# Kernel optimization log

Hardware: AMD Instinct MI355X
Metric: run time of the kernel (lower is better)

The kernel has to match this reference:

```python
import jax, jax.numpy as jnp
import numpy as np

N_NODES = 50000


def gcn_conv(x, W, b, src, dst, n):
    """PyG-style GCNConv: symmetric-normalized aggregation over A + I.
    x: [N, Fin], W: [Fin, Fout], b: [Fout], src/dst: [E] int edge endpoints.
    """
    h = x @ W  # [N, Fout]
    # degree with self-loops: deg[i] = 1 + in-degree(i)
    deg = jnp.zeros((n,), dtype=h.dtype).at[dst].add(1.0) + 1.0
    dinv = jax.lax.rsqrt(deg)  # deg^-1/2
    norm_e = dinv[src] * dinv[dst]  # [E]
    # message passing: sum_j norm_ij * h_j  (plus self-loop term deg_i^-1 * h_i)
    agg = jnp.zeros_like(h).at[dst].add(h[src] * norm_e[:, None])
    agg = agg + h * (dinv * dinv)[:, None]
    return agg + b


def setup_inputs() -> dict:
    key = jax.random.key(0)
    ks = jax.random.split(key, 9)
    N, F_in, H, C = N_NODES, 128, 64, 4
    E = 1600000
    node_features = jax.random.normal(ks[0], (N, F_in), dtype=jnp.float32)
    edge_index = jax.random.randint(ks[1], (2, E), 0, N, dtype=jnp.int32)
    s1 = 1.0 / np.sqrt(F_in)
    s2 = 1.0 / np.sqrt(H)
    W1 = jax.random.uniform(ks[2], (F_in, H), jnp.float32, -s1, s1)
    b1 = jax.random.uniform(ks[3], (H,), jnp.float32, -s1, s1)
    W2 = jax.random.uniform(ks[4], (H, H), jnp.float32, -s2, s2)
    b2 = jax.random.uniform(ks[5], (H,), jnp.float32, -s2, s2)
    W3 = jax.random.uniform(ks[6], (H, C), jnp.float32, -s2, s2)
    b3 = jax.random.uniform(ks[7], (C,), jnp.float32, -s2, s2)
    return {"node_features": node_features, "edge_index": edge_index,
            "W1": W1, "b1": b1, "W2": W2, "b2": b2, "W3": W3, "b3": b3}


def reference(node_features, edge_index, W1, b1, W2, b2, W3, b3):
    n = node_features.shape[0]
    src, dst = edge_index[0], edge_index[1]
    out = jax.nn.relu(gcn_conv(node_features, W1, b1, src, dst, n))
    # layer2 applied 7 times with SHARED weights (faithful to the source)
    for _ in range(7):
        out = jax.nn.relu(gcn_conv(out, W2, b2, src, dst, n))
    out = gcn_conv(out, W3, b3, src, dst, n)
    return jax.nn.softmax(out, axis=0)  # softmax over the node dimension (dim=0)
```

## Files before the change

kernel.cpp:

```cpp
#include <hip/hip_runtime.h>
#include <hip/hip_fp16.h>
#include <math.h>
#include <float.h>


#define NPART 8
#define BPP   104
#define T     4

typedef float f4 __attribute__((ext_vector_type(4)));


__global__ __launch_bounds__(256) void k_count(const int* __restrict__ src,
                                               const int* __restrict__ dst,
                                               unsigned* __restrict__ cnt,
                                               int E, int chunkS) {
    int e = blockIdx.x * 256 + threadIdx.x;
    if (e >= E) return;
    int d = dst[e];
    int t = src[e] / chunkS;
    atomicAdd(&cnt[d * T + t], 1u);
}

__global__ __launch_bounds__(256) void k_dinv(const int* __restrict__ rowt,
                                              float* __restrict__ dinv, int n) {
    int i = blockIdx.x * 256 + threadIdx.x;
    if (i < n) dinv[i] = rsqrtf(1.0f + (float)(rowt[i * T + T] - rowt[i * T]));
}


__global__ __launch_bounds__(256) void k_scan1(const unsigned* __restrict__ cnt,
                                               int* __restrict__ rowt,
                                               unsigned* __restrict__ bsum, int m) {
    __shared__ unsigned t[256];
    int i = blockIdx.x * 256 + threadIdx.x;
    unsigned v = (i < m) ? cnt[i] : 0u;
    t[threadIdx.x] = v;
    __syncthreads();
    #pragma unroll
    for (int off = 1; off < 256; off <<= 1) {
        unsigned u = (threadIdx.x >= (unsigned)off) ? t[threadIdx.x - off] : 0u;
        __syncthreads();
        t[threadIdx.x] += u;
        __syncthreads();
    }
    if (i < m) rowt[i] = (int)(t[threadIdx.x] - v);
    if (threadIdx.x == 255) bsum[blockIdx.x] = t[255];
}

__global__ __launch_bounds__(256) void k_scan2(unsigned* __restrict__ bsum,
                                               int* __restrict__ rowt,
                                               int nb, int m, int E) {
    __shared__ unsigned t[256];
    unsigned run = 0;
    for (int base = 0; base < nb; base += 256) {
        int i = base + threadIdx.x;
        unsigned v = (i < nb) ? bsum[i] : 0u;
        t[threadIdx.x] = v;
        __syncthreads();
        #pragma unroll
        for (int off = 1; off < 256; off <<= 1) {
            unsigned u = (threadIdx.x >= (unsigned)off) ? t[threadIdx.x - off] : 0u;
            __syncthreads();
            t[threadIdx.x] += u;
            __syncthreads();
        }
        if (i < nb) bsum[i] = run + t[threadIdx.x] - v;
        __syncthreads();
        run += t[255];
        __syncthreads();
    }
    if (threadIdx.x == 0) rowt[m] = E;
}

__global__ __launch_bounds__(256) void k_scan3(int* __restrict__ rowt,
                                               const unsigned* __restrict__ bsum, int m) {
    int i = blockIdx.x * 256 + threadIdx.x;
    if (i < m) rowt[i] += (int)bsum[blockIdx.x];
}


__global__ __launch_bounds__(256) void k_fill(const int* __restrict__ src,
                                              const int* __restrict__ dst,
                                              const int* __restrict__ rowt,
                                              unsigned* __restrict__ cursor,
                                              int* __restrict__ csr_src,
                                              int E, int chunk, int chunkS) {
    int part = blockIdx.x & (NPART - 1);
    int q = blockIdx.x >> 3;
    int lo = part * chunk, hi = lo + chunk;
    for (int e = q * 256 + threadIdx.x; e < E; e += 256 * BPP) {
        int d = dst[e];
        if (d >= lo && d < hi) {
            int s = src[e];
            int slot4 = d * T + s / chunkS;
            unsigned pos = atomicAdd(&cursor[slot4], 1u);
            csr_src[rowt[slot4] + (int)pos] = s;
        }
    }
}


__global__ __launch_bounds__(256) void k_gemm64_f32(const float* __restrict__ x,
                                                    const float* __restrict__ W,
                                                    const float* __restrict__ dinv,
                                                    __half* __restrict__ hs, int n) {
    __shared__ float Wl[128 * 64];
    {
        const f4* Wv = (const f4*)W;
        f4* Wlv = (f4*)Wl;
        for (int idx = threadIdx.x; idx < 128 * 16; idx += 256) Wlv[idx] = Wv[idx];
    }
    __syncthreads();
    int wave = threadIdx.x >> 6, lane = threadIdx.x & 63;
    int i0 = blockIdx.x * 16 + wave * 4;
    if (i0 >= n) return;
    if (i0 + 3 < n) {
        const f4* r0 = (const f4*)(x + (size_t)(i0 + 0) * 128);
        const f4* r1 = (const f4*)(x + (size_t)(i0 + 1) * 128);
        const f4* r2 = (const f4*)(x + (size_t)(i0 + 2) * 128);
        const f4* r3 = (const f4*)(x + (size_t)(i0 + 3) * 128);
        float a0 = 0.f, a1 = 0.f, a2 = 0.f, a3 = 0.f;
        #pragma unroll
        for (int k4 = 0; k4 < 32; ++k4) {
            f4 v0 = __builtin_nontemporal_load(&r0[k4]);
            f4 v1 = __builtin_nontemporal_load(&r1[k4]);
            f4 v2 = __builtin_nontemporal_load(&r2[k4]);
            f4 v3 = __builtin_nontemporal_load(&r3[k4]);
            float w0 = Wl[(k4 * 4 + 0) * 64 + lane];
            float w1 = Wl[(k4 * 4 + 1) * 64 + lane];
            float w2 = Wl[(k4 * 4 + 2) * 64 + lane];
            float w3 = Wl[(k4 * 4 + 3) * 64 + lane];
            a0 += v0.x * w0 + v0.y * w1 + v0.z * w2 + v0.w * w3;
            a1 += v1.x * w0 + v1.y * w1 + v1.z * w2 + v1.w * w3;
            a2 += v2.x * w0 + v2.y * w1 + v2.z * w2 + v2.w * w3;
            a3 += v3.x * w0 + v3.y * w1 + v3.z * w2 + v3.w * w3;
        }
        hs[(size_t)(i0 + 0) * 64 + lane] = __float2half(a0 * dinv[i0 + 0]);
        hs[(size_t)(i0 + 1) * 64 + lane] = __float2half(a1 * dinv[i0 + 1]);
        hs[(size_t)(i0 + 2) * 64 + lane] = __float2half(a2 * dinv[i0 + 2]);
        hs[(size_t)(i0 + 3) * 64 + lane] = __float2half(a3 * dinv[i0 + 3]);
    } else {
        for (int i = i0; i < n && i < i0 + 4; ++i) {
            const f4* r = (const f4*)(x + (size_t)i * 128);
            float acc = 0.f;
            #pragma unroll
            for (int k4 = 0; k4 < 32; ++k4) {
                f4 v = r[k4];
                acc += v.x * Wl[(k4 * 4 + 0) * 64 + lane];
                acc += v.y * Wl[(k4 * 4 + 1) * 64 + lane];
                acc += v.z * Wl[(k4 * 4 + 2) * 64 + lane];
                acc += v.w * Wl[(k4 * 4 + 3) * 64 + lane];
            }
            hs[(size_t)i * 64 + lane] = __float2half(acc * dinv[i]);
        }
    }
}


__global__ __launch_bounds__(256) void k_gemm64_f16(const __half* __restrict__ xh,
                                                    const float* __restrict__ W,
                                                    const float* __restrict__ dinv,
                                                    __half* __restrict__ hs, int n) {
    __shared__ float Wl[64 * 64];
    {
        const f4* Wv = (const f4*)W;
        f4* Wlv = (f4*)Wl;
        for (int idx = threadIdx.x; idx < 64 * 16; idx += 256) Wlv[idx] = Wv[idx];
    }
    __syncthreads();
    int wave = threadIdx.x >> 6, lane = threadIdx.x & 63;
    int i0 = blockIdx.x * 16 + wave * 4;
    if (i0 >= n) return;
    if (i0 + 3 < n) {
        const unsigned* r0 = (const unsigned*)(xh + (size_t)(i0 + 0) * 64);
        const unsigned* r1 = (const unsigned*)(xh + (size_t)(i0 + 1) * 64);
        const unsigned* r2 = (const unsigned*)(xh + (size_t)(i0 + 2) * 64);
        const unsigned* r3 = (const unsigned*)(xh + (size_t)(i0 + 3) * 64);
        float a0 = 0.f, a1 = 0.f, a2 = 0.f, a3 = 0.f;
        #pragma unroll
        for (int k2 = 0; k2 < 32; ++k2) {
            unsigned u0 = __builtin_nontemporal_load(&r0[k2]);
            unsigned u1 = __builtin_nontemporal_load(&r1[k2]);
            unsigned u2 = __builtin_nontemporal_load(&r2[k2]);
            unsigned u3 = __builtin_nontemporal_load(&r3[k2]);
            float w0 = Wl[(k2 * 2 + 0) * 64 + lane];
            float w1 = Wl[(k2 * 2 + 1) * 64 + lane];
            float2 v0 = __half22float2(*(__half2*)&u0);
            float2 v1 = __half22float2(*(__half2*)&u1);
            float2 v2 = __half22float2(*(__half2*)&u2);
            float2 v3 = __half22float2(*(__half2*)&u3);
            a0 += v0.x * w0 + v0.y * w1;
            a1 += v1.x * w0 + v1.y * w1;
            a2 += v2.x * w0 + v2.y * w1;
            a3 += v3.x * w0 + v3.y * w1;
        }
        hs[(size_t)(i0 + 0) * 64 + lane] = __float2half(a0 * dinv[i0 + 0]);
        hs[(size_t)(i0 + 1) * 64 + lane] = __float2half(a1 * dinv[i0 + 1]);
        hs[(size_t)(i0 + 2) * 64 + lane] = __float2half(a2 * dinv[i0 + 2]);
        hs[(size_t)(i0 + 3) * 64 + lane] = __float2half(a3 * dinv[i0 + 3]);
    } else {
        for (int i = i0; i < n && i < i0 + 4; ++i) {
            const __half2* r = (const __half2*)(xh + (size_t)i * 64);
            float acc = 0.f;
            #pragma unroll
            for (int k2 = 0; k2 < 32; ++k2) {
                float2 v = __half22float2(r[k2]);
                acc += v.x * Wl[(k2 * 2 + 0) * 64 + lane];
                acc += v.y * Wl[(k2 * 2 + 1) * 64 + lane];
            }
            hs[(size_t)i * 64 + lane] = __float2half(acc * dinv[i]);
        }
    }
}

__global__ __launch_bounds__(256) void k_gemm4(const __half* __restrict__ xh,
                                               const float* __restrict__ W,
                                               const float* __restrict__ dinv,
                                               float4* __restrict__ h4, int n) {
    __shared__ float Wl[256];
    for (int idx = threadIdx.x; idx < 256; idx += 256) Wl[idx] = W[idx];
    __syncthreads();
    int i = blockIdx.x * 256 + threadIdx.x;
    if (i >= n) return;
    const __half2* ar = (const __half2*)(xh + (size_t)i * 64);
    float a0 = 0.f, a1 = 0.f, a2 = 0.f, a3 = 0.f;
    #pragma unroll
    for (int k2 = 0; k2 < 32; ++k2) {
        float2 v = __half22float2(ar[k2]);
        int k = k2 * 2;
        a0 += v.x * Wl[k * 4 + 0] + v.y * Wl[(k + 1) * 4 + 0];
        a1 += v.x * Wl[k * 4 + 1] + v.y * Wl[(k + 1) * 4 + 1];
        a2 += v.x * Wl[k * 4 + 2] + v.y * Wl[(k + 1) * 4 + 2];
        a3 += v.x * Wl[k * 4 + 3] + v.y * Wl[(k + 1) * 4 + 3];
    }
    float di = dinv[i];
    h4[i] = make_float4(a0 * di, a1 * di, a2 * di, a3 * di);
}


__global__ __launch_bounds__(256) void k_agg64h(const __half* __restrict__ hs,
                                                const float* __restrict__ dinv,
                                                const int* __restrict__ rowt,
                                                const int* __restrict__ csr_src,
                                                const float* __restrict__ bias,
                                                __half* __restrict__ out, int n) {
    int wid = __builtin_amdgcn_readfirstlane((int)(threadIdx.x >> 6));
    int lane = threadIdx.x & 63;
    int gw = blockIdx.x * 4 + wid;
    if (gw >= n) return;
    float acc = __half2float(hs[(size_t)gw * 64 + lane]);
    int s = rowt[gw * T], e = rowt[gw * T + T];
    int slot = s;
    for (; slot + 16 <= e; slot += 16) {
        int idx[16];
        #pragma unroll
        for (int j = 0; j < 16; ++j) idx[j] = csr_src[slot + j];
        float v[16];
        #pragma unroll
        for (int j = 0; j < 16; ++j) v[j] = __half2float(hs[(size_t)idx[j] * 64 + lane]);
        float t0 = ((v[0] + v[1]) + (v[2] + v[3])) + ((v[4] + v[5]) + (v[6] + v[7]));
        float t1 = ((v[8] + v[9]) + (v[10] + v[11])) + ((v[12] + v[13]) + (v[14] + v[15]));
        acc += t0 + t1;
    }
    for (; slot + 4 <= e; slot += 4) {
        int i0 = csr_src[slot + 0];
        int i1 = csr_src[slot + 1];
        int i2 = csr_src[slot + 2];
        int i3 = csr_src[slot + 3];
        float v0 = __half2float(hs[(size_t)i0 * 64 + lane]);
        float v1 = __half2float(hs[(size_t)i1 * 64 + lane]);
        float v2 = __half2float(hs[(size_t)i2 * 64 + lane]);
        float v3 = __half2float(hs[(size_t)i3 * 64 + lane]);
        acc += (v0 + v1) + (v2 + v3);
    }
    for (; slot < e; ++slot)
        acc += __half2float(hs[(size_t)csr_src[slot] * 64 + lane]);
    acc = acc * dinv[gw] + bias[lane];
    out[(size_t)gw * 64 + lane] = __float2half(fmaxf(acc, 0.f));
}


__global__ __launch_bounds__(256) void k_agg4(const float4* __restrict__ h4,
                                              const float* __restrict__ dinv,
                                              const int* __restrict__ rowt,
                                              const int* __restrict__ csr_src,
                                              const float* __restrict__ b3,
                                              float4* __restrict__ z, int n) {
    int i = blockIdx.x * 256 + threadIdx.x;
    if (i >= n) return;
    float4 self = h4[i];
    float a0 = self.x, a1 = self.y, a2 = self.z, a3 = self.w;
    int s = rowt[i * T], e = rowt[i * T + T];
    int slot = s;
    for (; slot + 4 <= e; slot += 4) {
        int s0 = csr_src[slot + 0];
        int s1 = csr_src[slot + 1];
        int s2 = csr_src[slot + 2];
        int s3 = csr_src[slot + 3];
        float4 v0 = h4[s0], v1 = h4[s1], v2 = h4[s2], v3 = h4[s3];
        a0 += v0.x + v1.x + v2.x + v3.x;
        a1 += v0.y + v1.y + v2.y + v3.y;
        a2 += v0.z + v1.z + v2.z + v3.z;
        a3 += v0.w + v1.w + v2.w + v3.w;
    }
    for (; slot < e; ++slot) {
        float4 v = h4[csr_src[slot]];
        a0 += v.x; a1 += v.y; a2 += v.z; a3 += v.w;
    }
    float di = dinv[i];
    z[i] = make_float4(a0 * di + b3[0], a1 * di + b3[1],
                       a2 * di + b3[2], a3 * di + b3[3]);
}


__device__ inline unsigned encf(float f) {
    unsigned u = __float_as_uint(f);
    return (u & 0x80000000u) ? ~u : (u | 0x80000000u);
}
__device__ inline float decf(unsigned e) {
    return (e & 0x80000000u) ? __uint_as_float(e & 0x7FFFFFFFu) : __uint_as_float(~e);
}

__global__ __launch_bounds__(256) void k_max(const float4* __restrict__ z,
                                             unsigned* __restrict__ gmax, int n) {
    float m0 = -FLT_MAX, m1 = -FLT_MAX, m2 = -FLT_MAX, m3 = -FLT_MAX;
    for (int i = blockIdx.x * 256 + threadIdx.x; i < n; i += gridDim.x * 256) {
        float4 v = z[i];
        m0 = fmaxf(m0, v.x); m1 = fmaxf(m1, v.y);
        m2 = fmaxf(m2, v.z); m3 = fmaxf(m3, v.w);
    }
    #pragma unroll
    for (int off = 32; off; off >>= 1) {
        m0 = fmaxf(m0, __shfl_xor(m0, off));
        m1 = fmaxf(m1, __shfl_xor(m1, off));
        m2 = fmaxf(m2, __shfl_xor(m2, off));
        m3 = fmaxf(m3, __shfl_xor(m3, off));
    }
    if ((threadIdx.x & 63) == 0) {
        atomicMax(&gmax[0], encf(m0));
        atomicMax(&gmax[1], encf(m1));
        atomicMax(&gmax[2], encf(m2));
        atomicMax(&gmax[3], encf(m3));
    }
}

__global__ __launch_bounds__(256) void k_exp(const float4* __restrict__ z,
                                             float4* __restrict__ out,
                                             const unsigned* __restrict__ gmax,
                                             float* __restrict__ gsum, int n) {
    float M0 = decf(gmax[0]), M1 = decf(gmax[1]), M2 = decf(gmax[2]), M3 = decf(gmax[3]);
    float s0 = 0.f, s1 = 0.f, s2 = 0.f, s3 = 0.f;
    for (int i = blockIdx.x * 256 + threadIdx.x; i < n; i += gridDim.x * 256) {
        float4 v = z[i];
        float4 e;
        e.x = expf(v.x - M0); e.y = expf(v.y - M1);
        e.z = expf(v.z - M2); e.w = expf(v.w - M3);
        out[i] = e;
        s0 += e.x; s1 += e.y; s2 += e.z; s3 += e.w;
    }
    #pragma unroll
    for (int off = 32; off; off >>= 1) {
        s0 += __shfl_xor(s0, off);
        s1 += __shfl_xor(s1, off);
        s2 += __shfl_xor(s2, off);
        s3 += __shfl_xor(s3, off);
    }
    if ((threadIdx.x & 63) == 0) {
        atomicAdd(&gsum[0], s0);
        atomicAdd(&gsum[1], s1);
        atomicAdd(&gsum[2], s2);
        atomicAdd(&gsum[3], s3);
    }
}

__global__ __launch_bounds__(256) void k_norm(float4* __restrict__ out,
                                              const float* __restrict__ gsum, int n) {
    float r0 = 1.f / gsum[0], r1 = 1.f / gsum[1], r2 = 1.f / gsum[2], r3 = 1.f / gsum[3];
    for (int i = blockIdx.x * 256 + threadIdx.x; i < n; i += gridDim.x * 256) {
        float4 v = out[i];
        v.x *= r0; v.y *= r1; v.z *= r2; v.w *= r3;
        out[i] = v;
    }
}


extern "C" void kernel_launch(void* const* d_in, const int* in_sizes, int n_in,
                              void* d_out, int out_size, void* d_ws, size_t ws_size,
                              hipStream_t stream) {
    const float* x0 = (const float*)d_in[0];
    const int* ei = (const int*)d_in[1];
    const float* W1 = (const float*)d_in[2];
    const float* b1 = (const float*)d_in[3];
    const float* W2 = (const float*)d_in[4];
    const float* b2 = (const float*)d_in[5];
    const float* W3 = (const float*)d_in[6];
    const float* b3 = (const float*)d_in[7];

    const int n = in_sizes[0] / 128;
    const int E = in_sizes[1] / 2;
    const int* src = ei;
    const int* dst = ei + E;
    const int chunk = (n + NPART - 1) / NPART;
    const int chunkS = (n + T - 1) / T;
    const int m = n * T;

    char* ws = (char*)d_ws;
    size_t off = 0;
    auto alloc = [&](size_t bytes) -> void* {
        void* p = (void*)(ws + off);
        off = (off + bytes + 255) & ~(size_t)255;
        return p;
    };

    unsigned* cnt    = (unsigned*)alloc((size_t)m * 4);
    unsigned* cursor = (unsigned*)alloc((size_t)m * 4);
    unsigned* gmax   = (unsigned*)alloc(16);
    float*    gsum   = (float*)alloc(16);
    size_t zero_bytes = off;

    float* dinv      = (float*)alloc((size_t)n * 4);
    int*   rowt      = (int*)alloc((size_t)(m + 1) * 4);
    unsigned* bsum   = (unsigned*)alloc(1024 * 4);
    int*   csr_src   = (int*)alloc((size_t)E * 4);
    __half* hbuf     = (__half*)alloc((size_t)n * 64 * 2);
    __half* xbuf     = (__half*)alloc((size_t)n * 64 * 2);
    float4* h4buf    = (float4*)alloc((size_t)n * 16);
    float4* zbuf     = (float4*)alloc((size_t)n * 16);

    hipMemsetAsync(cnt, 0, zero_bytes, stream);

    const int nbN = (n + 255) / 256;
    const int nbE = (E + 255) / 256;
    const int nbM = (m + 255) / 256;

    k_count<<<nbE, 256, 0, stream>>>(src, dst, cnt, E, chunkS);
    k_scan1<<<nbM, 256, 0, stream>>>(cnt, rowt, bsum, m);
    k_scan2<<<1, 256, 0, stream>>>(bsum, rowt, nbM, m, E);
    k_scan3<<<nbM, 256, 0, stream>>>(rowt, bsum, m);
    k_dinv<<<nbN, 256, 0, stream>>>(rowt, dinv, n);
    k_fill<<<NPART * BPP, 256, 0, stream>>>(src, dst, rowt, cursor, csr_src, E, chunk, chunkS);

    const int nbG = (n + 15) / 16;
    const int nbA = (n + 3) / 4;

    k_gemm64_f32<<<nbG, 256, 0, stream>>>(x0, W1, dinv, hbuf, n);
    k_agg64h<<<nbA, 256, 0, stream>>>(hbuf, dinv, rowt, csr_src, b1, xbuf, n);

    for (int l = 0; l < 7; ++l) {
        k_gemm64_f16<<<nbG, 256, 0, stream>>>(xbuf, W2, dinv, hbuf, n);
        k_agg64h<<<nbA, 256, 0, stream>>>(hbuf, dinv, rowt, csr_src, b2, xbuf, n);
    }

    k_gemm4<<<nbN, 256, 0, stream>>>(xbuf, W3, dinv, h4buf, n);
    k_agg4<<<nbN, 256, 0, stream>>>(h4buf, dinv, rowt, csr_src, b3, zbuf, n);

    k_max<<<256, 256, 0, stream>>>(zbuf, gmax, n);
    k_exp<<<256, 256, 0, stream>>>(zbuf, (float4*)d_out, gmax, gsum, n);
    k_norm<<<256, 256, 0, stream>>>((float4*)d_out, gsum, n);
}
```

Measured before the change: 845.3 us.

## Compress CSR source indices to 16-bit pairs with even-padded segments

Stores the CSR neighbour indices as unsigned short instead of int, which halves the index traffic read in every aggregation pass. Each cell segment is padded to even length, and the pad slot points to an extra zero row at index n of the feature buffers. This lets the aggregation kernels read two indices per 32-bit load, and degree is now computed from the raw counts. The scheme relies on node ids fitting in 16 bits (N=50000) and adds a pad-fix kernel plus a zero-row kernel.

Measured after the change: 853.7 us. Within noise of the previous version (+1.0%).

```diff
diff --git a/kernel.cpp b/kernel.cpp
--- a/kernel.cpp
+++ b/kernel.cpp
@@ -22,10 +22,19 @@
     atomicAdd(&cnt[d * T + t], 1u);
 }
 
-__global__ __launch_bounds__(256) void k_dinv(const int* __restrict__ rowt,
+__global__ __launch_bounds__(256) void k_dinv(const unsigned* __restrict__ cnt,
                                               float* __restrict__ dinv, int n) {
     int i = blockIdx.x * 256 + threadIdx.x;
-    if (i < n) dinv[i] = rsqrtf(1.0f + (float)(rowt[i * T + T] - rowt[i * T]));
+    if (i < n) {
+        unsigned deg = cnt[i * T + 0] + cnt[i * T + 1] + cnt[i * T + 2] + cnt[i * T + 3];
+        dinv[i] = rsqrtf(1.0f + (float)deg);
+    }
+}
+
+__global__ __launch_bounds__(64) void k_zpad(__half* __restrict__ hs,
+                                             float4* __restrict__ h4, int n) {
+    hs[(size_t)n * 64 + threadIdx.x] = __float2half(0.f);
+    if (threadIdx.x == 0) h4[n] = make_float4(0.f, 0.f, 0.f, 0.f);
 }
 
 
@@ -34,7 +43,8 @@
                                                unsigned* __restrict__ bsum, int m) {
     __shared__ unsigned t[256];
     int i = blockIdx.x * 256 + threadIdx.x;
-    unsigned v = (i < m) ? cnt[i] : 0u;
+    unsigned v = 0;
+    if (i < m) { v = cnt[i]; v += (v & 1u); }
     t[threadIdx.x] = v;
     __syncthreads();
     #pragma unroll
@@ -50,7 +60,7 @@
 
 __global__ __launch_bounds__(256) void k_scan2(unsigned* __restrict__ bsum,
                                                int* __restrict__ rowt,
-                                               int nb, int m, int E) {
+                                               int nb, int m) {
     __shared__ unsigned t[256];
     unsigned run = 0;
     for (int base = 0; base < nb; base += 256) {
@@ -70,7 +80,7 @@
         run += t[255];
         __syncthreads();
     }
-    if (threadIdx.x == 0) rowt[m] = E;
+    if (threadIdx.x == 0) rowt[m] = (int)run;
 }
 
 __global__ __launch_bounds__(256) void k_scan3(int* __restrict__ rowt,
@@ -84,7 +94,7 @@
                                               const int* __restrict__ dst,
                                               const int* __restrict__ rowt,
                                               unsigned* __restrict__ cursor,
-                                              int* __restrict__ csr_src,
+                                              unsigned short* __restrict__ csr,
                                               int E, int chunk, int chunkS) {
     int part = blockIdx.x & (NPART - 1);
     int q = blockIdx.x >> 3;
@@ -93,11 +103,21 @@
         int d = dst[e];
         if (d >= lo && d < hi) {
             int s = src[e];
-            int slot4 = d * T + s / chunkS;
-            unsigned pos = atomicAdd(&cursor[slot4], 1u);
-            csr_src[rowt[slot4] + (int)pos] = s;
-        }
-    }
+            int cell = d * T + s / chunkS;
+            unsigned pos = atomicAdd(&cursor[cell], 1u);
+            csr[rowt[cell] + (int)pos] = (unsigned short)s;
+        }
+    }
+}
+
+__global__ __launch_bounds__(256) void k_padfix(const unsigned* __restrict__ cnt,
+                                                const int* __restrict__ rowt,
+                                                unsigned short* __restrict__ csr,
+                                                int m, int n) {
+    int i = blockIdx.x * 256 + threadIdx.x;
+    if (i >= m) return;
+    unsigned c = cnt[i];
+    if (c & 1u) csr[rowt[i] + (int)c] = (unsigned short)n;
 }
 
 
@@ -242,7 +262,7 @@
 __global__ __launch_bounds__(256) void k_agg64h(const __half* __restrict__ hs,
                                                 const float* __restrict__ dinv,
                                                 const int* __restrict__ rowt,
-                                                const int* __restrict__ csr_src,
+                                                const unsigned short* __restrict__ csr,
                                                 const float* __restrict__ bias,
                                                 __half* __restrict__ out, int n) {
     int wid = __builtin_amdgcn_readfirstlane((int)(threadIdx.x >> 6));
@@ -251,31 +271,28 @@
     if (gw >= n) return;
     float acc = __half2float(hs[(size_t)gw * 64 + lane]);
     int s = rowt[gw * T], e = rowt[gw * T + T];
-    int slot = s;
-    for (; slot + 16 <= e; slot += 16) {
-        int idx[16];
+    const unsigned* c32 = (const unsigned*)csr;
+    int p = s >> 1, pe = e >> 1;
+    for (; p + 8 <= pe; p += 8) {
+        unsigned pr[8];
         #pragma unroll
-        for (int j = 0; j < 16; ++j) idx[j] = csr_src[slot + j];
+        for (int j = 0; j < 8; ++j) pr[j] = c32[p + j];
         float v[16];
         #pragma unroll
-        for (int j = 0; j < 16; ++j) v[j] = __half2float(hs[(size_t)idx[j] * 64 + lane]);
+        for (int j = 0; j < 8; ++j) {
+            v[2 * j + 0] = __half2float(hs[(size_t)(pr[j] & 0xFFFFu) * 64 + lane]);
+            v[2 * j + 1] = __half2float(hs[(size_t)(pr[j] >> 16) * 64 + lane]);
+        }
         float t0 = ((v[0] + v[1]) + (v[2] + v[3])) + ((v[4] + v[5]) + (v[6] + v[7]));
         float t1 = ((v[8] + v[9]) + (v[10] + v[11])) + ((v[12] + v[13]) + (v[14] + v[15]));
         acc += t0 + t1;
     }
-    for (; slot + 4 <= e; slot += 4) {
-        int i0 = csr_src[slot + 0];
-        int i1 = csr_src[slot + 1];
-        int i2 = csr_src[slot + 2];
-        int i3 = csr_src[slot + 3];
-        float v0 = __half2float(hs[(size_t)i0 * 64 + lane]);
-        float v1 = __half2float(hs[(size_t)i1 * 64 + lane]);
-        float v2 = __half2float(hs[(size_t)i2 * 64 + lane]);
-        float v3 = __half2float(hs[(size_t)i3 * 64 + lane]);
-        acc += (v0 + v1) + (v2 + v3);
-    }
-    for (; slot < e; ++slot)
-        acc += __half2float(hs[(size_t)csr_src[slot] * 64 + lane]);
+    for (; p < pe; ++p) {
+        unsigned pr = c32[p];
+        float v0 = __half2float(hs[(size_t)(pr & 0xFFFFu) * 64 + lane]);
+        float v1 = __half2float(hs[(size_t)(pr >> 16) * 64 + lane]);
+        acc += v0 + v1;
+    }
     acc = acc * dinv[gw] + bias[lane];
     out[(size_t)gw * 64 + lane] = __float2half(fmaxf(acc, 0.f));
 }
@@ -284,7 +301,7 @@
 __global__ __launch_bounds__(256) void k_agg4(const float4* __restrict__ h4,
                                               const float* __restrict__ dinv,
                                               const int* __restrict__ rowt,
-                                              const int* __restrict__ csr_src,
+                                              const unsigned short* __restrict__ csr,
                                               const float* __restrict__ b3,
                                               float4* __restrict__ z, int n) {
     int i = blockIdx.x * 256 + threadIdx.x;
@@ -292,21 +309,22 @@
     float4 self = h4[i];
     float a0 = self.x, a1 = self.y, a2 = self.z, a3 = self.w;
     int s = rowt[i * T], e = rowt[i * T + T];
-    int slot = s;
-    for (; slot + 4 <= e; slot += 4) {
-        int s0 = csr_src[slot + 0];
-        int s1 = csr_src[slot + 1];
-        int s2 = csr_src[slot + 2];
-        int s3 = csr_src[slot + 3];
-        float4 v0 = h4[s0], v1 = h4[s1], v2 = h4[s2], v3 = h4[s3];
+    const unsigned* c32 = (const unsigned*)csr;
+    int p = s >> 1, pe = e >> 1;
+    for (; p + 2 <= pe; p += 2) {
+        unsigned pa = c32[p], pb = c32[p + 1];
+        float4 v0 = h4[pa & 0xFFFFu], v1 = h4[pa >> 16];
+        float4 v2 = h4[pb & 0xFFFFu], v3 = h4[pb >> 16];
         a0 += v0.x + v1.x + v2.x + v3.x;
         a1 += v0.y + v1.y + v2.y + v3.y;
         a2 += v0.z + v1.z + v2.z + v3.z;
         a3 += v0.w + v1.w + v2.w + v3.w;
     }
-    for (; slot < e; ++slot) {
-        float4 v = h4[csr_src[slot]];
-        a0 += v.x; a1 += v.y; a2 += v.z; a3 += v.w;
+    for (; p < pe; ++p) {
+        unsigned pr = c32[p];
+        float4 v0 = h4[pr & 0xFFFFu], v1 = h4[pr >> 16];
+        a0 += v0.x + v1.x; a1 += v0.y + v1.y;
+        a2 += v0.z + v1.z; a3 += v0.w + v1.w;
     }
     float di = dinv[i];
     z[i] = make_float4(a0 * di + b3[0], a1 * di + b3[1],
@@ -422,10 +440,10 @@
     float* dinv      = (float*)alloc((size_t)n * 4);
     int*   rowt      = (int*)alloc((size_t)(m + 1) * 4);
     unsigned* bsum   = (unsigned*)alloc(1024 * 4);
-    int*   csr_src   = (int*)alloc((size_t)E * 4);
-    __half* hbuf     = (__half*)alloc((size_t)n * 64 * 2);
+    unsigned short* csr = (unsigned short*)alloc(((size_t)E + m + 2) * 2);
+    __half* hbuf     = (__half*)alloc((size_t)(n + 1) * 64 * 2);
     __half* xbuf     = (__half*)alloc((size_t)n * 64 * 2);
-    float4* h4buf    = (float4*)alloc((size_t)n * 16);
+    float4* h4buf    = (float4*)alloc((size_t)(n + 1) * 16);
     float4* zbuf     = (float4*)alloc((size_t)n * 16);
 
     hipMemsetAsync(cnt, 0, zero_bytes, stream);
@@ -434,26 +452,28 @@
     const int nbE = (E + 255) / 256;
     const int nbM = (m + 255) / 256;
 
+    k_zpad<<<1, 64, 0, stream>>>(hbuf, h4buf, n);
     k_count<<<nbE, 256, 0, stream>>>(src, dst, cnt, E, chunkS);
     k_scan1<<<nbM, 256, 0, stream>>>(cnt, rowt, bsum, m);
-    k_scan2<<<1, 256, 0, stream>>>(bsum, rowt, nbM, m, E);
+    k_scan2<<<1, 256, 0, stream>>>(bsum, rowt, nbM, m);
     k_scan3<<<nbM, 256, 0, stream>>>(rowt, bsum, m);
-    k_dinv<<<nbN, 256, 0, stream>>>(rowt, dinv, n);
-    k_fill<<<NPART * BPP, 256, 0, stream>>>(src, dst, rowt, cursor, csr_src, E, chunk, chunkS);
+    k_dinv<<<nbN, 256, 0, stream>>>(cnt, dinv, n);
+    k_fill<<<NPART * BPP, 256, 0, stream>>>(src, dst, rowt, cursor, csr, E, chunk, chunkS);
+    k_padfix<<<nbM, 256, 0, stream>>>(cnt, rowt, csr, m, n);
 
     const int nbG = (n + 15) / 16;
     const int nbA = (n + 3) / 4;
 
     k_gemm64_f32<<<nbG, 256, 0, stream>>>(x0, W1, dinv, hbuf, n);
-    k_agg64h<<<nbA, 256, 0, stream>>>(hbuf, dinv, rowt, csr_src, b1, xbuf, n);
+    k_agg64h<<<nbA, 256, 0, stream>>>(hbuf, dinv, rowt, csr, b1, xbuf, n);
 
     for (int l = 0; l < 7; ++l) {
         k_gemm64_f16<<<nbG, 256, 0, stream>>>(xbuf, W2, dinv, hbuf, n);
-        k_agg64h<<<nbA, 256, 0, stream>>>(hbuf, dinv, rowt, csr_src, b2, xbuf, n);
+        k_agg64h<<<nbA, 256, 0, stream>>>(hbuf, dinv, rowt, csr, b2, xbuf, n);
     }
 
     k_gemm4<<<nbN, 256, 0, stream>>>(xbuf, W3, dinv, h4buf, n);
-    k_agg4<<<nbN, 256, 0, stream>>>(h4buf, dinv, rowt, csr_src, b3, zbuf, n);
+    k_agg4<<<nbN, 256, 0, stream>>>(h4buf, dinv, rowt, csr, b3, zbuf, n);
 
     k_max<<<256, 256, 0, stream>>>(zbuf, gmax, n);
     k_exp<<<256, 256, 0, stream>>>(zbuf, (float4*)d_out, gmax, gsum, n);
```
